# Kernel optimization log

Measured on AMD Instinct MI355X. Metric: run time of the kernel, lower is better.

Reference implementation:

```python
import jax, jax.numpy as jnp
import numpy as np

N_HEAD = 12

def setup_inputs() -> dict:
    key = jax.random.key(0)
    k1, k2, k3 = jax.random.split(key, 3)
    B, T, C = 8, 1024, 768
    x = jax.random.normal(k1, (B, T, C), dtype=jnp.float32)
    # torch nn.Linear weight layout: [out_features, in_features]
    W_attn = jax.random.normal(k2, (3 * C, C), dtype=jnp.float32) * 0.02
    b_attn = jax.random.normal(k3, (3 * C,), dtype=jnp.float32) * 0.02
    return {"x": x, "W_attn": W_attn, "b_attn": b_attn}

def reference(x, W_attn, b_attn):
    B, T, C = x.shape
    H = N_HEAD
    hs = C // H
    scale = 1.0 / jnp.sqrt(jnp.asarray(hs, x.dtype))
    # fused qkv projection: x @ W^T + b  -> [B, T, 3C]
    qkv = jnp.einsum('btc,oc->bto', x, W_attn) + b_attn
    qkv = qkv.reshape(B, T, 3, H, hs).transpose(2, 0, 3, 1, 4)  # [3, B, H, T, hs]
    q, k, v = qkv[0], qkv[1], qkv[2]
    scores = jnp.einsum('bhqd,bhkd->bhqk', q, k) * scale  # [B, H, T, T]
    causal = jnp.tril(jnp.ones((T, T), dtype=bool))
    # masked_fill(-inf) followed by ReLU == zero out masked positions after ReLU
    att = jnp.where(causal, jax.nn.relu(scores), jnp.zeros((), scores.dtype))
    y = jnp.einsum('bhqk,bhkd->bhqd', att, v)  # [B, H, T, hs]
    return y.transpose(0, 2, 1, 3).reshape(B, T, C)
```

## Files before the change

kernel.cpp:

```cpp
#include <hip/hip_runtime.h>
#include <hip/hip_bf16.h>
#include <stdint.h>

#define T_ 1024
#define C_ 768
#define H_ 12
#define HS 64

typedef __attribute__((ext_vector_type(8))) short bf16x8;
typedef __attribute__((ext_vector_type(4))) float f32x4;

#define GLOAD16(g, l) __builtin_amdgcn_global_load_lds( \
    (const __attribute__((address_space(1))) uint32_t*)(g), \
    (__attribute__((address_space(3))) uint32_t*)(l), 16, 0, 0)

__device__ __forceinline__ ushort f2b(float f) {
  uint32_t u = __builtin_bit_cast(uint32_t, f);
  u = (u + 0x7fffu + ((u >> 16) & 1u)) >> 16;
  return (ushort)u;
}

__global__ __launch_bounds__(256) void cvt_bf16(
    const float* __restrict__ x, const float* __restrict__ wt,
    ushort* __restrict__ xb, ushort* __restrict__ wb) {
  const int NX4 = 8192 * 768 / 4;
  const int NW4 = 2304 * 768 / 4;
  int i = blockIdx.x * 256 + threadIdx.x;
  int stride = gridDim.x * 256;
  for (int idx = i; idx < NX4; idx += stride) {
    float4 f = ((const float4*)x)[idx];
    ushort4 o;
    o.x = f2b(f.x); o.y = f2b(f.y); o.z = f2b(f.z); o.w = f2b(f.w);
    ((ushort4*)xb)[idx] = o;
  }
  for (int idx = i; idx < NW4; idx += stride) {
    float4 f = ((const float4*)wt)[idx];
    ushort4 o;
    o.x = f2b(f.x); o.y = f2b(f.y); o.z = f2b(f.z); o.w = f2b(f.w);
    ((ushort4*)wb)[idx] = o;
  }
}

__global__ __launch_bounds__(256) void qkv_gemm(
    const ushort* __restrict__ xb, const ushort* __restrict__ wb,
    const float* __restrict__ bias,
    ushort* __restrict__ qo, ushort* __restrict__ ko, ushort* __restrict__ vT) {
  __shared__ __align__(16) ushort smem[16384];
  const int tid = threadIdx.x, lane = tid & 63, w = tid >> 6;
  const int g = lane >> 4, l15 = lane & 15;
  const int m0 = blockIdx.y * 128, n0 = blockIdx.x * 128;
  const int wr = w >> 1, wc = w & 1;
  f32x4 acc[4][4] = {};

  const ushort* srcA[2];
  const ushort* srcB[2];
  int dstoff[2];
  #pragma unroll
  for (int c = 0; c < 2; ++c) {
    int p = (c * 4 + w) * 64 + lane;
    int row = p >> 2, s = p & 3;
    int sc = (s ^ ((row >> 1) & 3)) * 8;
    srcA[c] = xb + (size_t)(m0 + row) * 768 + sc;
    srcB[c] = wb + (size_t)(n0 + row) * 768 + sc;
    dstoff[c] = (c * 4 + w) * 1024;
  }

#define STAGE_G(buf, k0) do { \
    char* bb_ = (char*)smem + (buf) * 16384; \
    _Pragma("unroll") \
    for (int c_ = 0; c_ < 2; ++c_) { \
      GLOAD16(srcA[c_] + (k0), bb_ + dstoff[c_]); \
      GLOAD16(srcB[c_] + (k0), bb_ + 8192 + dstoff[c_]); \
    } \
  } while (0)

  int cur = 0;
  STAGE_G(0, 0);
  __syncthreads();
  #pragma unroll 2
  for (int kk = 0; kk < 24; ++kk) {
    if (kk < 23) STAGE_G(cur ^ 1, (kk + 1) * 32);
    const char* Ab = (const char*)smem + cur * 16384;
    const char* Bb = Ab + 8192;
    bf16x8 af[4], bfr[4];
    #pragma unroll
    for (int mi = 0; mi < 4; ++mi) {
      int r = wr * 64 + mi * 16 + l15;
      af[mi] = *(const bf16x8*)(Ab + r * 64 + ((g ^ ((r >> 1) & 3)) << 4));
    }
    #pragma unroll
    for (int ni = 0; ni < 4; ++ni) {
      int r = wc * 64 + ni * 16 + l15;
      bfr[ni] = *(const bf16x8*)(Bb + r * 64 + ((g ^ ((r >> 1) & 3)) << 4));
    }
    #pragma unroll
    for (int mi = 0; mi < 4; ++mi)
      #pragma unroll
      for (int ni = 0; ni < 4; ++ni)
        acc[mi][ni] = __builtin_amdgcn_mfma_f32_16x16x32_bf16(af[mi], bfr[ni], acc[mi][ni], 0, 0, 0);
    __syncthreads();
    cur ^= 1;
  }

  const int which = n0 / 768;
  if (which < 2) {
    ushort* outp = (which == 0) ? qo : ko;
    #pragma unroll
    for (int ni = 0; ni < 4; ++ni) {
      int n = n0 + wc * 64 + ni * 16 + l15;
      float bn = bias[n];
      int nin = n - which * 768;
      int h = nin >> 6, d = nin & 63;
      #pragma unroll
      for (int mi = 0; mi < 4; ++mi) {
        #pragma unroll
        for (int r = 0; r < 4; ++r) {
          int m = m0 + wr * 64 + mi * 16 + g * 4 + r;
          float val = acc[mi][ni][r] + bn;
          outp[((size_t)((m >> 10) * H_ + h) * T_ + (m & (T_ - 1))) * HS + d] = f2b(val);
        }
      }
    }
  } else {
    #pragma unroll
    for (int ni = 0; ni < 4; ++ni) {
      int n = n0 + wc * 64 + ni * 16 + l15;
      float bn = bias[n];
      int dl = wc * 64 + ni * 16 + l15;
      #pragma unroll
      for (int mi = 0; mi < 4; ++mi) {
        #pragma unroll
        for (int r = 0; r < 4; ++r) {
          int tl = wr * 64 + mi * 16 + g * 4 + r;
          *(ushort*)((char*)smem + dl * 256 + ((tl * 2) ^ ((dl & 7) << 4))) =
              f2b(acc[mi][ni][r] + bn);
        }
      }
    }
    __syncthreads();
    const int b = m0 >> 10, t0base = m0 & 1023;
    #pragma unroll
    for (int c = 0; c < 8; ++c) {
      int p = c * 256 + tid;
      int dl = p >> 4, tch = p & 15;
      uint4 val = *(const uint4*)((const char*)smem + dl * 256 + ((tch * 16) ^ ((dl & 7) << 4)));
      int nin = n0 + dl - 1536;
      int h = nin >> 6, dd = nin & 63;
      *(uint4*)(vT + (((size_t)(b * H_ + h) * HS + dd) << 10) + t0base + tch * 8) = val;
    }
  }
}

__global__ __launch_bounds__(256) void attn_relu(
    const ushort* __restrict__ q, const ushort* __restrict__ k,
    const ushort* __restrict__ vT, float* __restrict__ out) {
  __shared__ __align__(16) ushort smem[20480];
  const int tid = threadIdx.x, lane = tid & 63, w = tid >> 6;
  const int g = lane >> 4, l15 = lane & 15;
  const int bh = blockIdx.x, qt = 15 - blockIdx.y;
  const int q0 = qt * 64;
  const size_t base = (size_t)bh * (T_ * HS);
  const int qrow = w * 16 + l15;

  bf16x8 qf[2];
  #pragma unroll
  for (int kd = 0; kd < 2; ++kd)
    qf[kd] = *(const bf16x8*)(q + base + (size_t)(q0 + qrow) * HS + (kd * 4 + g) * 8);

  int rowS[2], scS[2], dstoff[2];
  #pragma unroll
  for (int c = 0; c < 2; ++c) {
    int p = (c * 4 + w) * 64 + lane;
    rowS[c] = p >> 3;
    scS[c] = ((p & 7) ^ (rowS[c] & 7)) * 8;
    dstoff[c] = (c * 4 + w) * 1024;
  }

#define STAGE_KV(buf, kt) do { \
    char* bb_ = (char*)smem + (buf) * 16384; \
    _Pragma("unroll") \
    for (int c_ = 0; c_ < 2; ++c_) { \
      GLOAD16(k + base + (size_t)((kt) * 64 + rowS[c_]) * HS + scS[c_], bb_ + dstoff[c_]); \
      GLOAD16(vT + base + (size_t)rowS[c_] * T_ + (kt) * 64 + scS[c_], bb_ + 8192 + dstoff[c_]); \
    } \
  } while (0)

  f32x4 yacc[4] = {};
  const int nkt = qt + 1;
  int cur = 0;
  STAGE_KV(0, 0);
  __syncthreads();
  for (int kt = 0; kt < nkt; ++kt) {
    if (kt + 1 < nkt) STAGE_KV(cur ^ 1, kt + 1);
    const char* Kb = (const char*)smem + cur * 16384;
    const char* Vb = Kb + 8192;
    char* Pb = (char*)smem + 32768;

    f32x4 sacc[4] = {};
    #pragma unroll
    for (int kd = 0; kd < 2; ++kd) {
      #pragma unroll
      for (int nt = 0; nt < 4; ++nt) {
        int kr = nt * 16 + l15;
        bf16x8 kf = *(const bf16x8*)(Kb + kr * 128 + (((kd * 4 + g) ^ (kr & 7)) << 4));
        sacc[nt] = __builtin_amdgcn_mfma_f32_16x16x32_bf16(qf[kd], kf, sacc[nt], 0, 0, 0);
      }
    }

    #pragma unroll
    for (int nt = 0; nt < 4; ++nt) {
      int kj = kt * 64 + nt * 16 + l15;
      #pragma unroll
      for (int r = 0; r < 4; ++r) {
        int i = w * 16 + g * 4 + r;
        float sv = sacc[nt][r] * 0.125f;
        float pv = (kj <= q0 + i) ? fmaxf(sv, 0.0f) : 0.0f;
        *(ushort*)(Pb + i * 128 + (((nt * 16 + l15) * 2) ^ ((i & 7) << 4))) = f2b(pv);
      }
    }

    bf16x8 pf[2], vf[2][4];
    #pragma unroll
    for (int kj2 = 0; kj2 < 2; ++kj2) {
      pf[kj2] = *(const bf16x8*)(Pb + qrow * 128 + (((kj2 * 4 + g) ^ (qrow & 7)) << 4));
      #pragma unroll
      for (int nt = 0; nt < 4; ++nt) {
        int vr = nt * 16 + l15;
        vf[kj2][nt] = *(const bf16x8*)(Vb + vr * 128 + (((kj2 * 4 + g) ^ (vr & 7)) << 4));
      }
    }
    #pragma unroll
    for (int kj2 = 0; kj2 < 2; ++kj2)
      #pragma unroll
      for (int nt = 0; nt < 4; ++nt)
        yacc[nt] = __builtin_amdgcn_mfma_f32_16x16x32_bf16(pf[kj2], vf[kj2][nt], yacc[nt], 0, 0, 0);

    __syncthreads();
    cur ^= 1;
  }

  const int bb = bh / H_, hh = bh % H_;
  #pragma unroll
  for (int nt = 0; nt < 4; ++nt) {
    #pragma unroll
    for (int r = 0; r < 4; ++r) {
      int t = q0 + w * 16 + g * 4 + r;
      int col = hh * HS + nt * 16 + l15;
      out[(size_t)(bb * T_ + t) * C_ + col] = yacc[nt][r];
    }
  }
}

extern "C" void kernel_launch(void* const* d_in, const int* in_sizes, int n_in,
                              void* d_out, int out_size, void* d_ws, size_t ws_size,
                              hipStream_t stream) {
  const float* x    = (const float*)d_in[0];
  const float* W    = (const float*)d_in[1];
  const float* bias = (const float*)d_in[2];
  float* out = (float*)d_out;

  char* ws = (char*)d_ws;
  ushort* xb = (ushort*)ws;
  ushort* wb = (ushort*)(ws + 12582912);
  ushort* qb = (ushort*)(ws + 16121856);
  ushort* kb = (ushort*)(ws + 28704768);
  ushort* vT = (ushort*)(ws + 41287680);

  cvt_bf16<<<2048, 256, 0, stream>>>(x, W, xb, wb);
  qkv_gemm<<<dim3(18, 64), 256, 0, stream>>>(xb, wb, bias, qb, kb, vT);
  attn_relu<<<dim3(96, 16), 256, 0, stream>>>(qb, kb, vT, out);
}
```

Measured before the change: 162.8 us.

## Triple-buffer GEMM and attention loads, remap blocks across XCDs, coalesce Q/K stores

Both the QKV GEMM and the causal attention loop move from double to triple-buffered async global-to-LDS loads. Explicit vmcnt waits plus a raw barrier let two tiles stay in flight while the current one is computed. Grids are flattened to 1D and remapped so consecutive blocks spread across the 8 XCDs, wave priority is raised around MFMA bursts, and the Q/K epilogue is staged through LDS so global writes are 16-byte and coalesced. The cost is more LDS per block, which can lower occupancy, and a manual wait count that must match the number of loads issued per stage.

```diff
diff --git a/kernel.cpp b/kernel.cpp
--- a/kernel.cpp
+++ b/kernel.cpp
@@ -13,6 +13,8 @@
 #define GLOAD16(g, l) __builtin_amdgcn_global_load_lds( \
     (const __attribute__((address_space(1))) uint32_t*)(g), \
     (__attribute__((address_space(3))) uint32_t*)(l), 16, 0, 0)
+
+#define WAITCNT_VM(n) asm volatile("s_waitcnt vmcnt(" #n ")" ::: "memory")
 
 __device__ __forceinline__ ushort f2b(float f) {
   uint32_t u = __builtin_bit_cast(uint32_t, f);
@@ -45,10 +47,12 @@
     const ushort* __restrict__ xb, const ushort* __restrict__ wb,
     const float* __restrict__ bias,
     ushort* __restrict__ qo, ushort* __restrict__ ko, ushort* __restrict__ vT) {
-  __shared__ __align__(16) ushort smem[16384];
+  __shared__ __align__(16) char smem[49152];
   const int tid = threadIdx.x, lane = tid & 63, w = tid >> 6;
   const int g = lane >> 4, l15 = lane & 15;
-  const int m0 = blockIdx.y * 128, n0 = blockIdx.x * 128;
+  const int id = blockIdx.x;
+  const int wg = (id & 7) * 144 + (id >> 3);
+  const int m0 = (wg / 18) * 128, n0 = (wg % 18) * 128;
   const int wr = w >> 1, wc = w & 1;
   f32x4 acc[4][4] = {};
 
@@ -65,74 +69,91 @@
     dstoff[c] = (c * 4 + w) * 1024;
   }
 
-#define STAGE_G(buf, k0) do { \
-    char* bb_ = (char*)smem + (buf) * 16384; \
+#define STAGE_G(bb_, k0) do { \
     _Pragma("unroll") \
     for (int c_ = 0; c_ < 2; ++c_) { \
-      GLOAD16(srcA[c_] + (k0), bb_ + dstoff[c_]); \
-      GLOAD16(srcB[c_] + (k0), bb_ + 8192 + dstoff[c_]); \
+      GLOAD16(srcA[c_] + (k0), (bb_) + dstoff[c_]); \
+      GLOAD16(srcB[c_] + (k0), (bb_) + 8192 + dstoff[c_]); \
     } \
   } while (0)
 
-  int cur = 0;
-  STAGE_G(0, 0);
+#define GEMM_COMPUTE(cb_) do { \
+    bf16x8 af[4], bfr[4]; \
+    _Pragma("unroll") \
+    for (int mi = 0; mi < 4; ++mi) { \
+      int r_ = wr * 64 + mi * 16 + l15; \
+      af[mi] = *(const bf16x8*)((cb_) + r_ * 64 + ((g ^ ((r_ >> 1) & 3)) << 4)); \
+    } \
+    _Pragma("unroll") \
+    for (int ni = 0; ni < 4; ++ni) { \
+      int r_ = wc * 64 + ni * 16 + l15; \
+      bfr[ni] = *(const bf16x8*)((cb_) + 8192 + r_ * 64 + ((g ^ ((r_ >> 1) & 3)) << 4)); \
+    } \
+    __builtin_amdgcn_s_setprio(1); \
+    _Pragma("unroll") \
+    for (int mi = 0; mi < 4; ++mi) \
+      _Pragma("unroll") \
+      for (int ni = 0; ni < 4; ++ni) \
+        acc[mi][ni] = __builtin_amdgcn_mfma_f32_16x16x32_bf16(af[mi], bfr[ni], acc[mi][ni], 0, 0, 0); \
+    __builtin_amdgcn_s_setprio(0); \
+  } while (0)
+
+  STAGE_G(smem, 0);
+  STAGE_G(smem + 16384, 32);
+  char* cptr = smem;
+  char* sptr = smem + 32768;
+  for (int kk = 0; kk < 23; ++kk) {
+    WAITCNT_VM(4);
+    __builtin_amdgcn_s_barrier();
+    if (kk < 22) STAGE_G(sptr, (kk + 2) * 32);
+    GEMM_COMPUTE(cptr);
+    cptr += 16384; if (cptr == smem + 49152) cptr = smem;
+    sptr += 16384; if (sptr == smem + 49152) sptr = smem;
+  }
+  WAITCNT_VM(0);
+  __builtin_amdgcn_s_barrier();
+  GEMM_COMPUTE(cptr);
   __syncthreads();
-  #pragma unroll 2
-  for (int kk = 0; kk < 24; ++kk) {
-    if (kk < 23) STAGE_G(cur ^ 1, (kk + 1) * 32);
-    const char* Ab = (const char*)smem + cur * 16384;
-    const char* Bb = Ab + 8192;
-    bf16x8 af[4], bfr[4];
-    #pragma unroll
-    for (int mi = 0; mi < 4; ++mi) {
-      int r = wr * 64 + mi * 16 + l15;
-      af[mi] = *(const bf16x8*)(Ab + r * 64 + ((g ^ ((r >> 1) & 3)) << 4));
-    }
-    #pragma unroll
-    for (int ni = 0; ni < 4; ++ni) {
-      int r = wc * 64 + ni * 16 + l15;
-      bfr[ni] = *(const bf16x8*)(Bb + r * 64 + ((g ^ ((r >> 1) & 3)) << 4));
-    }
-    #pragma unroll
-    for (int mi = 0; mi < 4; ++mi)
-      #pragma unroll
-      for (int ni = 0; ni < 4; ++ni)
-        acc[mi][ni] = __builtin_amdgcn_mfma_f32_16x16x32_bf16(af[mi], bfr[ni], acc[mi][ni], 0, 0, 0);
-    __syncthreads();
-    cur ^= 1;
-  }
 
   const int which = n0 / 768;
   if (which < 2) {
     ushort* outp = (which == 0) ? qo : ko;
     #pragma unroll
     for (int ni = 0; ni < 4; ++ni) {
-      int n = n0 + wc * 64 + ni * 16 + l15;
-      float bn = bias[n];
-      int nin = n - which * 768;
-      int h = nin >> 6, d = nin & 63;
+      float bn = bias[n0 + wc * 64 + ni * 16 + l15];
+      int nl = wc * 64 + ni * 16 + l15;
       #pragma unroll
       for (int mi = 0; mi < 4; ++mi) {
         #pragma unroll
         for (int r = 0; r < 4; ++r) {
-          int m = m0 + wr * 64 + mi * 16 + g * 4 + r;
-          float val = acc[mi][ni][r] + bn;
-          outp[((size_t)((m >> 10) * H_ + h) * T_ + (m & (T_ - 1))) * HS + d] = f2b(val);
+          int ml = wr * 64 + mi * 16 + g * 4 + r;
+          *(ushort*)(smem + ml * 256 + ((nl * 2) ^ ((ml & 7) << 4))) =
+              f2b(acc[mi][ni][r] + bn);
         }
       }
     }
+    __syncthreads();
+    #pragma unroll
+    for (int c = 0; c < 8; ++c) {
+      int p = c * 256 + tid;
+      int ml = p >> 4, nch = p & 15;
+      uint4 val = *(const uint4*)(smem + ml * 256 + ((nch * 16) ^ ((ml & 7) << 4)));
+      int m = m0 + ml;
+      int nin = n0 + nch * 8 - which * 768;
+      int h = nin >> 6, d = nin & 63;
+      *(uint4*)(outp + ((size_t)((m >> 10) * H_ + h) * T_ + (m & (T_ - 1))) * HS + d) = val;
+    }
   } else {
     #pragma unroll
     for (int ni = 0; ni < 4; ++ni) {
-      int n = n0 + wc * 64 + ni * 16 + l15;
-      float bn = bias[n];
+      float bn = bias[n0 + wc * 64 + ni * 16 + l15];
       int dl = wc * 64 + ni * 16 + l15;
       #pragma unroll
       for (int mi = 0; mi < 4; ++mi) {
         #pragma unroll
         for (int r = 0; r < 4; ++r) {
           int tl = wr * 64 + mi * 16 + g * 4 + r;
-          *(ushort*)((char*)smem + dl * 256 + ((tl * 2) ^ ((dl & 7) << 4))) =
+          *(ushort*)(smem + dl * 256 + ((tl * 2) ^ ((dl & 7) << 4))) =
               f2b(acc[mi][ni][r] + bn);
         }
       }
@@ -143,7 +164,7 @@
     for (int c = 0; c < 8; ++c) {
       int p = c * 256 + tid;
       int dl = p >> 4, tch = p & 15;
-      uint4 val = *(const uint4*)((const char*)smem + dl * 256 + ((tch * 16) ^ ((dl & 7) << 4)));
+      uint4 val = *(const uint4*)(smem + dl * 256 + ((tch * 16) ^ ((dl & 7) << 4)));
       int nin = n0 + dl - 1536;
       int h = nin >> 6, dd = nin & 63;
       *(uint4*)(vT + (((size_t)(b * H_ + h) * HS + dd) << 10) + t0base + tch * 8) = val;
@@ -154,10 +175,13 @@
 __global__ __launch_bounds__(256) void attn_relu(
     const ushort* __restrict__ q, const ushort* __restrict__ k,
     const ushort* __restrict__ vT, float* __restrict__ out) {
-  __shared__ __align__(16) ushort smem[20480];
+  __shared__ __align__(16) char smem[57344];
   const int tid = threadIdx.x, lane = tid & 63, w = tid >> 6;
   const int g = lane >> 4, l15 = lane & 15;
-  const int bh = blockIdx.x, qt = 15 - blockIdx.y;
+  const int id = blockIdx.x;
+  const int wg = (id & 7) * 192 + (id >> 3);
+  const int bh = wg >> 4;
+  const int qt = 15 - (wg & 15);
   const int q0 = qt * 64;
   const size_t base = (size_t)bh * (T_ * HS);
   const int qrow = w * 16 + l15;
@@ -176,68 +200,78 @@
     dstoff[c] = (c * 4 + w) * 1024;
   }
 
-#define STAGE_KV(buf, kt) do { \
-    char* bb_ = (char*)smem + (buf) * 16384; \
+#define STAGE_KV(bb_, kt) do { \
     _Pragma("unroll") \
     for (int c_ = 0; c_ < 2; ++c_) { \
-      GLOAD16(k + base + (size_t)((kt) * 64 + rowS[c_]) * HS + scS[c_], bb_ + dstoff[c_]); \
-      GLOAD16(vT + base + (size_t)rowS[c_] * T_ + (kt) * 64 + scS[c_], bb_ + 8192 + dstoff[c_]); \
+      GLOAD16(k + base + (size_t)((kt) * 64 + rowS[c_]) * HS + scS[c_], (bb_) + dstoff[c_]); \
+      GLOAD16(vT + base + (size_t)rowS[c_] * T_ + (kt) * 64 + scS[c_], (bb_) + 8192 + dstoff[c_]); \
     } \
   } while (0)
 
   f32x4 yacc[4] = {};
+  char* const Pb = smem + 49152;
+
+#define ATTN_COMPUTE(cb_, kt) do { \
+    const char* Kb = (cb_); \
+    const char* Vb = (cb_) + 8192; \
+    f32x4 sacc[4] = {}; \
+    __builtin_amdgcn_s_setprio(1); \
+    _Pragma("unroll") \
+    for (int kd = 0; kd < 2; ++kd) { \
+      _Pragma("unroll") \
+      for (int nt = 0; nt < 4; ++nt) { \
+        int kr = nt * 16 + l15; \
+        bf16x8 kf = *(const bf16x8*)(Kb + kr * 128 + (((kd * 4 + g) ^ (kr & 7)) << 4)); \
+        sacc[nt] = __builtin_amdgcn_mfma_f32_16x16x32_bf16(qf[kd], kf, sacc[nt], 0, 0, 0); \
+      } \
+    } \
+    __builtin_amdgcn_s_setprio(0); \
+    _Pragma("unroll") \
+    for (int nt = 0; nt < 4; ++nt) { \
+      int kj = (kt) * 64 + nt * 16 + l15; \
+      _Pragma("unroll") \
+      for (int r = 0; r < 4; ++r) { \
+        int i_ = w * 16 + g * 4 + r; \
+        float sv = sacc[nt][r] * 0.125f; \
+        float pv = (kj <= q0 + i_) ? fmaxf(sv, 0.0f) : 0.0f; \
+        *(ushort*)(Pb + i_ * 128 + (((nt * 16 + l15) * 2) ^ ((i_ & 7) << 4))) = f2b(pv); \
+      } \
+    } \
+    bf16x8 pf[2], vf[2][4]; \
+    _Pragma("unroll") \
+    for (int kj2 = 0; kj2 < 2; ++kj2) { \
+      pf[kj2] = *(const bf16x8*)(Pb + qrow * 128 + (((kj2 * 4 + g) ^ (qrow & 7)) << 4)); \
+      _Pragma("unroll") \
+      for (int nt = 0; nt < 4; ++nt) { \
+        int vr = nt * 16 + l15; \
+        vf[kj2][nt] = *(const bf16x8*)(Vb + vr * 128 + (((kj2 * 4 + g) ^ (vr & 7)) << 4)); \
+      } \
+    } \
+    __builtin_amdgcn_s_setprio(1); \
+    _Pragma("unroll") \
+    for (int kj2 = 0; kj2 < 2; ++kj2) \
+      _Pragma("unroll") \
+      for (int nt = 0; nt < 4; ++nt) \
+        yacc[nt] = __builtin_amdgcn_mfma_f32_16x16x32_bf16(pf[kj2], vf[kj2][nt], yacc[nt], 0, 0, 0); \
+    __builtin_amdgcn_s_setprio(0); \
+  } while (0)
+
   const int nkt = qt + 1;
-  int cur = 0;
-  STAGE_KV(0, 0);
-  __syncthreads();
-  for (int kt = 0; kt < nkt; ++kt) {
-    if (kt + 1 < nkt) STAGE_KV(cur ^ 1, kt + 1);
-    const char* Kb = (const char*)smem + cur * 16384;
-    const char* Vb = Kb + 8192;
-    char* Pb = (char*)smem + 32768;
-
-    f32x4 sacc[4] = {};
-    #pragma unroll
-    for (int kd = 0; kd < 2; ++kd) {
-      #pragma unroll
-      for (int nt = 0; nt < 4; ++nt) {
-        int kr = nt * 16 + l15;
-        bf16x8 kf = *(const bf16x8*)(Kb + kr * 128 + (((kd * 4 + g) ^ (kr & 7)) << 4));
-        sacc[nt] = __builtin_amdgcn_mfma_f32_16x16x32_bf16(qf[kd], kf, sacc[nt], 0, 0, 0);
-      }
-    }
-
-    #pragma unroll
-    for (int nt = 0; nt < 4; ++nt) {
-      int kj = kt * 64 + nt * 16 + l15;
-      #pragma unroll
-      for (int r = 0; r < 4; ++r) {
-        int i = w * 16 + g * 4 + r;
-        float sv = sacc[nt][r] * 0.125f;
-        float pv = (kj <= q0 + i) ? fmaxf(sv, 0.0f) : 0.0f;
-        *(ushort*)(Pb + i * 128 + (((nt * 16 + l15) * 2) ^ ((i & 7) << 4))) = f2b(pv);
-      }
-    }
-
-    bf16x8 pf[2], vf[2][4];
-    #pragma unroll
-    for (int kj2 = 0; kj2 < 2; ++kj2) {
-      pf[kj2] = *(const bf16x8*)(Pb + qrow * 128 + (((kj2 * 4 + g) ^ (qrow & 7)) << 4));
-      #pragma unroll
-      for (int nt = 0; nt < 4; ++nt) {
-        int vr = nt * 16 + l15;
-        vf[kj2][nt] = *(const bf16x8*)(Vb + vr * 128 + (((kj2 * 4 + g) ^ (vr & 7)) << 4));
-      }
-    }
-    #pragma unroll
-    for (int kj2 = 0; kj2 < 2; ++kj2)
-      #pragma unroll
-      for (int nt = 0; nt < 4; ++nt)
-        yacc[nt] = __builtin_amdgcn_mfma_f32_16x16x32_bf16(pf[kj2], vf[kj2][nt], yacc[nt], 0, 0, 0);
-
-    __syncthreads();
-    cur ^= 1;
-  }
+  STAGE_KV(smem, 0);
+  if (nkt > 1) STAGE_KV(smem + 16384, 1);
+  char* cptr = smem;
+  char* sptr = smem + 32768;
+  for (int kt = 0; kt < nkt - 1; ++kt) {
+    WAITCNT_VM(4);
+    __builtin_amdgcn_s_barrier();
+    if (kt + 2 < nkt) STAGE_KV(sptr, kt + 2);
+    ATTN_COMPUTE(cptr, kt);
+    cptr += 16384; if (cptr == smem + 49152) cptr = smem;
+    sptr += 16384; if (sptr == smem + 49152) sptr = smem;
+  }
+  WAITCNT_VM(0);
+  __builtin_amdgcn_s_barrier();
+  ATTN_COMPUTE(cptr, nkt - 1);
 
   const int bb = bh / H_, hh = bh % H_;
   #pragma unroll
@@ -267,6 +301,6 @@
   ushort* vT = (ushort*)(ws + 41287680);
 
   cvt_bf16<<<2048, 256, 0, stream>>>(x, W, xb, wb);
-  qkv_gemm<<<dim3(18, 64), 256, 0, stream>>>(xb, wb, bias, qb, kb, vT);
-  attn_relu<<<dim3(96, 16), 256, 0, stream>>>(qb, kb, vT, out);
-}
+  qkv_gemm<<<1152, 256, 0, stream>>>(xb, wb, bias, qb, kb, vT);
+  attn_relu<<<1536, 256, 0, stream>>>(qb, kb, vT, out);
+}
```

After: 166.7 us. +2.4%, slower.
